# Kernel optimization log

Hardware: AMD Instinct MI355X
Metric: run time of the kernel (lower is better)

Reference implementation:

```python
import jax, jax.numpy as jnp
import numpy as np
import math

B, N, F = 16, 1024, 2048


def setup_inputs() -> dict:
    key = jax.random.key(0)
    k_t, k_y = jax.random.split(key)
    # sorted time samples in [0, 100) per batch row
    t = jnp.sort(jax.random.uniform(k_t, (B, N), dtype=jnp.float32) * 100.0, axis=-1)
    y = jax.random.normal(k_y, (B, N), dtype=jnp.float32)
    mask = jnp.ones((B, N), dtype=jnp.float32)
    # monotonically increasing frequency grid (torch.diff in norm requires this)
    freqs = jnp.linspace(1e-5, 5.0, F, dtype=jnp.float32)
    return {"t": t, "y": y, "mask": mask, "freqs": freqs}


def reference(t, y, mask, freqs):
    # t, y, mask: (B, N); freqs: (F,)
    two_pi = 2.0 * math.pi
    omega = two_pi * freqs  # (F,)
    w = omega[None, :, None]          # (1, F, 1)
    tb = t[:, None, :]                # (B, 1, N)
    mb = mask[:, None, :]             # (B, 1, N)
    yb = y[:, None, :]                # (B, 1, N)

    # --- stage 1: tau per (batch, freq) ---
    two_wt = 2.0 * w * tb             # (B, F, N)
    s_sum = jnp.sum(jnp.sin(two_wt) * mb, axis=-1)  # (B, F)
    c_sum = jnp.sum(jnp.cos(two_wt) * mb, axis=-1)  # (B, F)
    tau = jnp.arctan2(s_sum, c_sum) / (2.0 * omega)  # (B, F)

    # --- stage 2: power ---
    wt_tau = w * (tb - tau[:, :, None])  # (B, F, N)
    cos_term = jnp.cos(wt_tau) * mb
    sin_term = jnp.sin(wt_tau) * mb
    p_cos = jnp.sum(yb * cos_term, axis=-1) ** 2 / (jnp.sum(cos_term * cos_term, axis=-1) + 1e-10)
    p_sin = jnp.sum(yb * sin_term, axis=-1) ** 2 / (jnp.sum(sin_term * sin_term, axis=-1) + 1e-10)
    p = 0.5 * (p_cos + p_sin)  # (B, F)

    # --- FAP weighting ---
    m = p.shape[-1]
    fap = 1.0 - (1.0 - jnp.exp(-p)) ** m
    p = p * (1.0 / (fap + 1e-5))

    # --- trapezoidal normalization over the freq grid ---
    df = jnp.diff(freqs)  # (F-1,)
    integral = jnp.sum(0.5 * (p[:, :-1] + p[:, 1:]) * df, axis=-1) + 1e-10  # (B,)
    return p / integral[:, None]
```

## Files before the change

### kernel.cpp

```cpp
#include <hip/hip_runtime.h>
#include <math.h>

#define B_ 16
#define N_ 1024
#define F_ 2048
#define FPB 32
#define SLICES 8
#define NS (N_ / SLICES)

__global__ __launch_bounds__(256) void ls_power_kernel(
    const float* __restrict__ t,
    const float* __restrict__ y,
    const float* __restrict__ mask,
    const float* __restrict__ freqs,
    float* __restrict__ p_out)
{
    const int tid   = threadIdx.x;
    const int fi    = tid & (FPB - 1);
    const int slice = tid >> 5;
    const int b     = blockIdx.y;
    const int f     = blockIdx.x * FPB + fi;

    __shared__ __align__(16) float sh_t[N_];
    __shared__ __align__(16) float sh_y[N_];
    __shared__ __align__(16) float sh_m[N_];
    __shared__ float red[SLICES][4][FPB];

    {
        const float4* t4 = (const float4*)(t    + b * N_);
        const float4* y4 = (const float4*)(y    + b * N_);
        const float4* m4 = (const float4*)(mask + b * N_);
        ((float4*)sh_t)[tid] = t4[tid];
        ((float4*)sh_y)[tid] = y4[tid];
        ((float4*)sh_m)[tid] = m4[tid];
    }

    const float freq  = freqs[f];
    const float omega = 6.28318530717958647692f * freq;
    const float f2    = 2.0f * freq;

    __syncthreads();

    float s_sum = 0.f, c_sum = 0.f;
    const int n0 = slice * NS;
#pragma unroll 8
    for (int n = n0; n < n0 + NS; ++n) {
        float tn = sh_t[n], mn = sh_m[n];
        float ph = f2 * tn;
        float pe = __builtin_fmaf(f2, tn, -ph);
        float r  = __builtin_amdgcn_fractf(ph) + pe;
        float s  = __builtin_amdgcn_sinf(r);
        float c  = __builtin_amdgcn_cosf(r);
        s_sum = __builtin_fmaf(s, mn, s_sum);
        c_sum = __builtin_fmaf(c, mn, c_sum);
    }
    red[slice][0][fi] = s_sum;
    red[slice][1][fi] = c_sum;
    __syncthreads();

    float S = 0.f, C = 0.f;
#pragma unroll
    for (int k = 0; k < SLICES; ++k) { S += red[k][0][fi]; C += red[k][1][fi]; }
    const float tau = atan2f(S, C) / (2.0f * omega);
    __syncthreads();

    float yc = 0.f, ys = 0.f, cc = 0.f, ss = 0.f;
#pragma unroll 8
    for (int n = n0; n < n0 + NS; ++n) {
        float tn = sh_t[n], mn = sh_m[n], yn = sh_y[n];
        float d  = tn - tau;
        float ph = freq * d;
        float pe = __builtin_fmaf(freq, d, -ph);
        float r  = __builtin_amdgcn_fractf(ph) + pe;
        float s  = __builtin_amdgcn_sinf(r) * mn;
        float c  = __builtin_amdgcn_cosf(r) * mn;
        yc = __builtin_fmaf(yn, c, yc);
        ys = __builtin_fmaf(yn, s, ys);
        cc = __builtin_fmaf(c, c, cc);
        ss = __builtin_fmaf(s, s, ss);
    }
    red[slice][0][fi] = yc;
    red[slice][1][fi] = ys;
    red[slice][2][fi] = cc;
    red[slice][3][fi] = ss;
    __syncthreads();

    if (slice == 0) {
        float YC = 0.f, YS = 0.f, CC = 0.f, SS = 0.f;
#pragma unroll
        for (int k = 0; k < SLICES; ++k) {
            YC += red[k][0][fi];
            YS += red[k][1][fi];
            CC += red[k][2][fi];
            SS += red[k][3][fi];
        }
        float p_cos = (YC * YC) / (CC + 1e-10f);
        float p_sin = (YS * YS) / (SS + 1e-10f);
        float p = 0.5f * (p_cos + p_sin);

        float fap = 1.0f - powf(1.0f - expf(-p), 2048.0f);
        p = p * (1.0f / (fap + 1e-5f));

        p_out[b * F_ + f] = p;
    }
}

__global__ __launch_bounds__(256) void ls_norm_kernel(
    const float* __restrict__ freqs,
    float* __restrict__ p)
{
    const int b   = blockIdx.x;
    const int tid = threadIdx.x;
    float* __restrict__ pb = p + b * F_;

    float local = 0.0f;
    for (int j = tid; j < F_ - 1; j += 256) {
        float df = freqs[j + 1] - freqs[j];
        local += 0.5f * (pb[j] + pb[j + 1]) * df;
    }

    __shared__ float sred[256];
    sred[tid] = local;
    __syncthreads();
    for (int o = 128; o > 0; o >>= 1) {
        if (tid < o) sred[tid] += sred[tid + o];
        __syncthreads();
    }
    const float integral = sred[0] + 1e-10f;

#pragma unroll
    for (int k = 0; k < F_ / 256; ++k) {
        int j = tid + k * 256;
        pb[j] = pb[j] / integral;
    }
}

extern "C" void kernel_launch(void* const* d_in, const int* in_sizes, int n_in,
                              void* d_out, int out_size, void* d_ws, size_t ws_size,
                              hipStream_t stream) {
    const float* t     = (const float*)d_in[0];
    const float* y     = (const float*)d_in[1];
    const float* mask  = (const float*)d_in[2];
    const float* freqs = (const float*)d_in[3];
    float* out = (float*)d_out;

    dim3 grid1(F_ / FPB, B_);
    ls_power_kernel<<<grid1, 256, 0, stream>>>(t, y, mask, freqs, out);
    ls_norm_kernel<<<B_, 256, 0, stream>>>(freqs, out);
}
```

Measured before the change: 86.23 us.

## Drop shared-memory staging, read inputs as uniform float4 loads, enlarge blocks

The kernel no longer stages t, y and mask in LDS. Each 64-lane wavefront maps to one slice, so its addresses are wave-uniform (readfirstlane), and it reads float4 chunks straight from global memory. Blocks grow to 1024 threads (64 freqs × 16 slices), and the error-compensation term is dropped from the stage-1 phase reduction. This removes the LDS fill, one barrier and LDS read traffic, but relies on cache-served broadcast loads and lowers the phase precision in stage 1.

```diff
diff --git a/kernel.cpp b/kernel.cpp
--- a/kernel.cpp
+++ b/kernel.cpp
@@ -4,11 +4,12 @@
 #define B_ 16
 #define N_ 1024
 #define F_ 2048
-#define FPB 32
-#define SLICES 8
+#define FPB 64
+#define SLICES 16
 #define NS (N_ / SLICES)
+#define NC (NS / 4)
 
-__global__ __launch_bounds__(256) void ls_power_kernel(
+__global__ __launch_bounds__(1024) void ls_power_kernel(
     const float* __restrict__ t,
     const float* __restrict__ y,
     const float* __restrict__ mask,
@@ -17,42 +18,36 @@
 {
     const int tid   = threadIdx.x;
     const int fi    = tid & (FPB - 1);
-    const int slice = tid >> 5;
+    const int slice = tid >> 6;
     const int b     = blockIdx.y;
     const int f     = blockIdx.x * FPB + fi;
-
-    __shared__ __align__(16) float sh_t[N_];
-    __shared__ __align__(16) float sh_y[N_];
-    __shared__ __align__(16) float sh_m[N_];
-    __shared__ float red[SLICES][4][FPB];
-
-    {
-        const float4* t4 = (const float4*)(t    + b * N_);
-        const float4* y4 = (const float4*)(y    + b * N_);
-        const float4* m4 = (const float4*)(mask + b * N_);
-        ((float4*)sh_t)[tid] = t4[tid];
-        ((float4*)sh_y)[tid] = y4[tid];
-        ((float4*)sh_m)[tid] = m4[tid];
-    }
 
     const float freq  = freqs[f];
     const float omega = 6.28318530717958647692f * freq;
     const float f2    = 2.0f * freq;
 
-    __syncthreads();
+    const int c0 = __builtin_amdgcn_readfirstlane(b * (N_ / 4) + slice * NC);
+    const float4* __restrict__ t4 = (const float4*)t;
+    const float4* __restrict__ y4 = (const float4*)y;
+    const float4* __restrict__ m4 = (const float4*)mask;
+
+    __shared__ float red[SLICES][4][FPB];
 
     float s_sum = 0.f, c_sum = 0.f;
-    const int n0 = slice * NS;
-#pragma unroll 8
-    for (int n = n0; n < n0 + NS; ++n) {
-        float tn = sh_t[n], mn = sh_m[n];
-        float ph = f2 * tn;
-        float pe = __builtin_fmaf(f2, tn, -ph);
-        float r  = __builtin_amdgcn_fractf(ph) + pe;
-        float s  = __builtin_amdgcn_sinf(r);
-        float c  = __builtin_amdgcn_cosf(r);
-        s_sum = __builtin_fmaf(s, mn, s_sum);
-        c_sum = __builtin_fmaf(c, mn, c_sum);
+#pragma unroll 4
+    for (int ch = 0; ch < NC; ++ch) {
+        float4 tv = t4[c0 + ch];
+        float4 mv = m4[c0 + ch];
+#pragma unroll
+        for (int k = 0; k < 4; ++k) {
+            float tn = (&tv.x)[k];
+            float mn = (&mv.x)[k];
+            float r  = __builtin_amdgcn_fractf(f2 * tn);
+            float s  = __builtin_amdgcn_sinf(r);
+            float c  = __builtin_amdgcn_cosf(r);
+            s_sum = __builtin_fmaf(s, mn, s_sum);
+            c_sum = __builtin_fmaf(c, mn, c_sum);
+        }
     }
     red[slice][0][fi] = s_sum;
     red[slice][1][fi] = c_sum;
@@ -65,19 +60,27 @@
     __syncthreads();
 
     float yc = 0.f, ys = 0.f, cc = 0.f, ss = 0.f;
-#pragma unroll 8
-    for (int n = n0; n < n0 + NS; ++n) {
-        float tn = sh_t[n], mn = sh_m[n], yn = sh_y[n];
-        float d  = tn - tau;
-        float ph = freq * d;
-        float pe = __builtin_fmaf(freq, d, -ph);
-        float r  = __builtin_amdgcn_fractf(ph) + pe;
-        float s  = __builtin_amdgcn_sinf(r) * mn;
-        float c  = __builtin_amdgcn_cosf(r) * mn;
-        yc = __builtin_fmaf(yn, c, yc);
-        ys = __builtin_fmaf(yn, s, ys);
-        cc = __builtin_fmaf(c, c, cc);
-        ss = __builtin_fmaf(s, s, ss);
+#pragma unroll 4
+    for (int ch = 0; ch < NC; ++ch) {
+        float4 tv = t4[c0 + ch];
+        float4 yv = y4[c0 + ch];
+        float4 mv = m4[c0 + ch];
+#pragma unroll
+        for (int k = 0; k < 4; ++k) {
+            float tn = (&tv.x)[k];
+            float yn = (&yv.x)[k];
+            float mn = (&mv.x)[k];
+            float d  = tn - tau;
+            float ph = freq * d;
+            float pe = __builtin_fmaf(freq, d, -ph);
+            float r  = __builtin_amdgcn_fractf(ph) + pe;
+            float s  = __builtin_amdgcn_sinf(r) * mn;
+            float c  = __builtin_amdgcn_cosf(r) * mn;
+            yc = __builtin_fmaf(yn, c, yc);
+            ys = __builtin_fmaf(yn, s, ys);
+            cc = __builtin_fmaf(c, c, cc);
+            ss = __builtin_fmaf(s, s, ss);
+        }
     }
     red[slice][0][fi] = yc;
     red[slice][1][fi] = ys;
@@ -145,6 +148,6 @@
     float* out = (float*)d_out;
 
     dim3 grid1(F_ / FPB, B_);
-    ls_power_kernel<<<grid1, 256, 0, stream>>>(t, y, mask, freqs, out);
+    ls_power_kernel<<<grid1, 1024, 0, stream>>>(t, y, mask, freqs, out);
     ls_norm_kernel<<<B_, 256, 0, stream>>>(freqs, out);
 }
```

After: 84.14 us. 1.02x faster.
